# Optimization experiments

Hardware: AMD Instinct MI355X
Metric: run time of the kernel (lower is better)

## Reference

```python
import jax, jax.numpy as jnp
import numpy as np
from jax.scipy.special import logsumexp

N, K, D = 131072, 256, 32


def setup_inputs() -> dict:
    key = jax.random.key(0)
    k1, k2, k3 = jax.random.split(key, 3)
    points = jax.random.normal(k1, (N, D), dtype=jnp.float32)
    centers = jax.random.uniform(k2, (K, D), dtype=jnp.float32)
    # well-conditioned inverse-sqrt covariances (original used 15*I; scaled to
    # avoid float32 overflow in sqrt(det(covs_inv)) for D=32)
    covs_inv_sqrt = (0.5 * jnp.broadcast_to(jnp.eye(D, dtype=jnp.float32), (K, D, D))
                     + 0.02 * jax.random.normal(k3, (K, D, D), dtype=jnp.float32))
    weights = jnp.ones((K,), dtype=jnp.float32)
    threshold = jnp.zeros((1,), dtype=jnp.float32)
    return {"points": points, "centers": centers,
            "covs_inv_sqrt": covs_inv_sqrt, "weights": weights,
            "threshold": threshold}


def reference(points, centers, covs_inv_sqrt, weights, threshold):
    # refresh(): equal_clusters=True branch
    w = jnp.abs(weights)
    center_prs = w / (w.sum() + 1e-30)                       # [K]
    covs_inv = jnp.einsum('kde,kfe->kdf', covs_inv_sqrt, covs_inv_sqrt)  # [K,D,D]
    coefs = center_prs * jnp.sqrt(jnp.linalg.det(covs_inv))  # [K]

    # pairwise weighted sqdist: q_ij = (x_i - c_j)^T A_j (x_i - c_j)
    B = covs_inv.reshape(K, D * D)                           # [K, D*D]
    X2 = (points[:, :, None] * points[:, None, :]).reshape(N, D * D)  # [N, D*D]
    t_xAx = X2 @ B.T                                         # [N, K]
    m = jnp.einsum('kde,ke->kd', covs_inv, centers)          # A_j c_j, [K,D]
    t_xAc = points @ m.T                                     # [N, K]
    t_cAc = jnp.einsum('kd,kd->k', m, centers)               # [K]
    d_ij = -0.5 * (t_xAx - 2.0 * t_xAc + t_cAc[None, :])     # [N, K]

    # weighted logsumexp over centers, then subtract threshold
    ll = logsumexp(d_ij, axis=1, b=coefs[None, :])           # [N]
    return ll[:, None] - threshold[0]                        # [N, 1]
```

## Files before the change

kernel.cpp:

```cpp
#include <hip/hip_runtime.h>
#include <hip/hip_fp16.h>
#include <math.h>

#define NPTS 131072
#define KCOMP 256
#define DIM 32
#define KF 608
#define PSIF_BYTES 311296
#define WS_NEED (PSIF_BYTES + KCOMP * 4)

typedef _Float16 f16x8 __attribute__((ext_vector_type(8)));
typedef __attribute__((ext_vector_type(16))) float f32x16;

constexpr int L4c(int d) { return ((32 - d + 3) / 4) * 4; }
constexpr int PfxC(int d) { int s = 0; for (int i = 0; i < d; ++i) s += L4c(i); return s; }
constexpr int rowOfC(int p) { int d = 0; while (d < 31 && PfxC(d + 1) <= p) ++d; return d; }
constexpr int dOfC(int p) { return (p >= 576) ? -1 : rowOfC(p); }
constexpr int f0OfC(int p) {
    return (p >= 576) ? (p - 576) : ((rowOfC(p) & ~3) + (p - PfxC(rowOfC(p))));
}

__device__ __forceinline__ unsigned short f2h(float v) {
    __half h = __float2half(v);
    return __builtin_bit_cast(unsigned short, h);
}

__global__ __launch_bounds__(256) void gmm_pre(
    const float* __restrict__ S,
    const float* __restrict__ centers,
    const float* __restrict__ weights,
    unsigned short* __restrict__ PsiF,
    float* __restrict__ kc2)
{
    __shared__ float Sl[DIM][DIM + 1];
    __shared__ float As[DIM][DIM + 1];
    __shared__ float cl[DIM], ml[DIM];
    __shared__ float red[256];

    const int k = blockIdx.x, tid = threadIdx.x;

    for (int idx = tid; idx < DIM * DIM; idx += 256)
        Sl[idx >> 5][idx & 31] = S[(size_t)k * DIM * DIM + idx];
    if (tid < DIM) cl[tid] = centers[k * DIM + tid];
    __syncthreads();

    for (int idx = tid; idx < DIM * DIM; idx += 256) {
        const int d = idx >> 5, f = idx & 31;
        float a = 0.f;
#pragma unroll
        for (int e = 0; e < DIM; ++e) a = fmaf(Sl[d][e], Sl[f][e], a);
        As[d][f] = a;
    }
    __syncthreads();

    if (tid < DIM) {
        float mv = 0.f;
#pragma unroll
        for (int f = 0; f < DIM; ++f) mv = fmaf(As[tid][f], cl[f], mv);
        ml[tid] = mv;
    }
    __syncthreads();

    for (int p = tid; p < KF; p += 256) {
        float val;
        if (p < 576) {
            int d = 0, pr = 0;
            while (true) {
                const int len = ((32 - d + 3) >> 2) << 2;
                if (pr + len > p) break;
                pr += len; ++d;
            }
            const int f = (d & ~3) + (p - pr);
            val = (f < d) ? 0.f : ((f == d) ? -0.5f * As[d][d] : -As[d][f]);
        } else {
            val = ml[p - 576];
        }
        const int c = p >> 6, kk = p & 63;
        const int s = kk >> 4, qq = (kk >> 3) & 1, j = kk & 7;
        const int ct = k >> 5, ll = qq * 32 + (k & 31);
        const int g = c * 2048 + (s * 8 + ct) * 64 + ll;
        PsiF[(size_t)g * 8 + j] = f2h(val);
    }

    red[tid] = fabsf(weights[tid]);
    __syncthreads();
    for (int off = 128; off > 0; off >>= 1) {
        if (tid < off) red[tid] += red[tid + off];
        __syncthreads();
    }
    const float wsum = red[0];

    for (int j = 0; j < DIM - 1; ++j) {
        const float inv = 1.0f / As[j][j];
        for (int idx = tid; idx < DIM * DIM; idx += 256) {
            const int r = idx >> 5, c = idx & 31;
            if (r > j && c > j)
                As[r][c] = fmaf(-As[r][j] * inv, As[j][c], As[r][c]);
        }
        __syncthreads();
    }

    if (tid < DIM) red[tid] = __logf(As[tid][tid]);
    __syncthreads();
    if (tid == 0) {
        float sl = 0.f;
        for (int j = 0; j < DIM; ++j) sl += red[j];
        float cac = 0.f;
        for (int d2 = 0; d2 < DIM; ++d2) cac = fmaf(ml[d2], cl[d2], cac);
        kc2[k] = __logf(fabsf(weights[k])) - __logf(wsum + 1e-30f)
               + 0.5f * sl - 0.5f * cac;
    }
}

__device__ __forceinline__ unsigned pkmul(unsigned a, unsigned b) {
    __half2 r = __builtin_bit_cast(__half2, a) * __builtin_bit_cast(__half2, b);
    return __builtin_bit_cast(unsigned, r);
}

template<int PA, int PB>
__device__ __forceinline__ void quadProd(const unsigned (&xp)[16], bool hi,
                                         unsigned& o0, unsigned& o1) {
    constexpr int dA = dOfC(PA), fA = f0OfC(PA);
    constexpr int dB = dOfC(PB), fB = f0OfC(PB);
    const unsigned p0 = hi ? xp[(fB >> 1) + 0] : xp[(fA >> 1) + 0];
    const unsigned p1 = hi ? xp[(fB >> 1) + 1] : xp[(fA >> 1) + 1];
    if constexpr (dA < 0) {
        o0 = p0; o1 = p1;
    } else {
        const unsigned sA = __builtin_amdgcn_perm(xp[dA >> 1], xp[dA >> 1],
                                (dA & 1) ? 0x03020302u : 0x01000100u);
        const unsigned sB = __builtin_amdgcn_perm(xp[dB >> 1], xp[dB >> 1],
                                (dB & 1) ? 0x03020302u : 0x01000100u);
        const unsigned ss = (dA == dB) ? sA : (hi ? sB : sA);
        o0 = pkmul(ss, p0); o1 = pkmul(ss, p1);
    }
}

template<int C, int S>
__device__ __forceinline__ uint4 genA(const unsigned (&xp)[16], bool hi) {
    constexpr int P = C * 64 + S * 16;
    uint4 u;
    quadProd<P,     P + 8 >(xp, hi, u.x, u.y);
    quadProd<P + 4, P + 12>(xp, hi, u.z, u.w);
    return u;
}

template<int ST>
__device__ __forceinline__ void doStep(
    const unsigned (&xp0)[16], const unsigned (&xp1)[16],
    uint4 (&bf)[2][4], f32x16 (&acc)[2][4],
    const uint4* __restrict__ pb, bool hi)
{
    constexpr int C = (ST < 36) ? ST / 4 : 9;
    constexpr int S = (ST < 36) ? ST % 4 : ST - 36;

    if constexpr (ST < 37) {
        constexpr int Cn = (ST + 1 < 36) ? (ST + 1) / 4 : 9;
        constexpr int Sn = (ST + 1 < 36) ? (ST + 1) % 4 : ST + 1 - 36;
#pragma unroll
        for (int ct = 0; ct < 4; ++ct)
            bf[(ST + 1) & 1][ct] = pb[Cn * 2048 + Sn * 512 + ct * 64];
    }

    const uint4 a0 = genA<C, S>(xp0, hi);
    const uint4 a1 = genA<C, S>(xp1, hi);
#pragma unroll
    for (int ct = 0; ct < 4; ++ct) {
        const f16x8 b  = __builtin_bit_cast(f16x8, bf[ST & 1][ct]);
        acc[0][ct] = __builtin_amdgcn_mfma_f32_32x32x16_f16(
                         __builtin_bit_cast(f16x8, a0), b, acc[0][ct], 0, 0, 0);
        acc[1][ct] = __builtin_amdgcn_mfma_f32_32x32x16_f16(
                         __builtin_bit_cast(f16x8, a1), b, acc[1][ct], 0, 0, 0);
    }
}

template<int ST>
__device__ __forceinline__ void runSteps(
    const unsigned (&xp0)[16], const unsigned (&xp1)[16],
    uint4 (&bf)[2][4], f32x16 (&acc)[2][4],
    const uint4* __restrict__ pb, bool hi)
{
    doStep<ST>(xp0, xp1, bf, acc, pb, hi);
    if constexpr (ST < 37) runSteps<ST + 1>(xp0, xp1, bf, acc, pb, hi);
}

__global__ __launch_bounds__(256, 2) void gmm_mfma(
    const float* __restrict__ points,
    const unsigned short* __restrict__ PsiF,
    const float* __restrict__ kc2,
    const float* __restrict__ thr,
    float* __restrict__ out)
{
    __shared__ float sPm[128][2], sPs[128][2];

    const int t = threadIdx.x;
    const int w = t >> 6, l = t & 63;
    const int rh = w >> 1, ch = w & 1;
    const bool hi = (l >> 5) != 0;

    unsigned xp0[16], xp1[16];
    {
        const size_t r0 = (size_t)blockIdx.x * 128 + rh * 64 + (l & 31);
        const float4* pxa = (const float4*)(points + r0 * DIM);
        const float4* pxb = (const float4*)(points + (r0 + 32) * DIM);
#pragma unroll
        for (int i = 0; i < 8; ++i) {
            float4 va = pxa[i], vb = pxb[i];
            xp0[2*i+0] = __builtin_bit_cast(unsigned, __floats2half2_rn(va.x, va.y));
            xp0[2*i+1] = __builtin_bit_cast(unsigned, __floats2half2_rn(va.z, va.w));
            xp1[2*i+0] = __builtin_bit_cast(unsigned, __floats2half2_rn(vb.x, vb.y));
            xp1[2*i+1] = __builtin_bit_cast(unsigned, __floats2half2_rn(vb.z, vb.w));
        }
    }

    const uint4* pb = (const uint4*)PsiF + ch * 256 + l;

    f32x16 acc[2][4];
#pragma unroll
    for (int a = 0; a < 2; ++a)
#pragma unroll
        for (int c = 0; c < 4; ++c)
#pragma unroll
            for (int r = 0; r < 16; ++r) acc[a][c][r] = 0.f;

    uint4 bf[2][4];
#pragma unroll
    for (int ct = 0; ct < 4; ++ct) bf[0][ct] = pb[ct * 64];

    runSteps<0>(xp0, xp1, bf, acc, pb, hi);

    float kcv[4];
#pragma unroll
    for (int ct = 0; ct < 4; ++ct) kcv[ct] = kc2[(ch * 4 + ct) * 32 + (l & 31)];

#pragma unroll
    for (int rt = 0; rt < 2; ++rt) {
#pragma unroll
        for (int rg = 0; rg < 16; ++rg) {
            float v0 = acc[rt][0][rg] + kcv[0];
            float v1 = acc[rt][1][rg] + kcv[1];
            float v2 = acc[rt][2][rg] + kcv[2];
            float v3 = acc[rt][3][rg] + kcv[3];
            float m = fmaxf(fmaxf(v0, v1), fmaxf(v2, v3));
#pragma unroll
            for (int mask = 1; mask < 32; mask <<= 1)
                m = fmaxf(m, __shfl_xor(m, mask, 64));
            float sv = __expf(v0 - m) + __expf(v1 - m)
                     + __expf(v2 - m) + __expf(v3 - m);
#pragma unroll
            for (int mask = 1; mask < 32; mask <<= 1)
                sv += __shfl_xor(sv, mask, 64);
            if ((l & 31) == 0) {
                const int R = rh * 64 + rt * 32 + (rg & 3) + 8 * (rg >> 2) + 4 * (l >> 5);
                sPm[R][ch] = m; sPs[R][ch] = sv;
            }
        }
    }
    __syncthreads();

    if (t < 128) {
        const float m0 = sPm[t][0], m1 = sPm[t][1];
        const float M = fmaxf(m0, m1);
        const float Sv = sPs[t][0] * __expf(m0 - M) + sPs[t][1] * __expf(m1 - M);
        out[(size_t)blockIdx.x * 128 + t] = M + __logf(Sv) - thr[0];
    }
}

extern "C" void kernel_launch(void* const* d_in, const int* in_sizes, int n_in,
                              void* d_out, int out_size, void* d_ws, size_t ws_size,
                              hipStream_t stream) {
    const float* points  = (const float*)d_in[0];
    const float* centers = (const float*)d_in[1];
    const float* covs    = (const float*)d_in[2];
    const float* weights = (const float*)d_in[3];
    const float* thr     = (const float*)d_in[4];
    float* out = (float*)d_out;

    unsigned short* PsiF = (unsigned short*)d_ws;
    float* kc2 = (float*)((char*)d_ws + PSIF_BYTES);

    gmm_pre<<<KCOMP, 256, 0, stream>>>(covs, centers, weights, PsiF, kc2);
    gmm_mfma<<<NPTS / 128, 256, 0, stream>>>(points, PsiF, kc2, thr, out);
}
```

Measured before the change: 155.3 us.

## Repartition MFMA warp tiling to 4 row tiles x 2 component tiles per wave

Changes the per-wave tiling so each of the 4 waves covers all 128 rows (4 row tiles) and 64 components (2 column tiles), instead of 64 rows x 128 components. Each wave now generates the on-the-fly x-outer-product A fragments for 4 row tiles and loads half as many B fragments, and B prefetch deepens from double to triple buffering two steps ahead. The aim is to cut global B traffic per wave and hide load latency better. In exchange, A-fragment generation ALU work per wave doubles, more registers go to x data, and the cross-wave logsumexp merge now spans 4 partials.

```diff
diff --git a/kernel.cpp b/kernel.cpp
--- a/kernel.cpp
+++ b/kernel.cpp
@@ -147,41 +147,43 @@
 
 template<int ST>
 __device__ __forceinline__ void doStep(
-    const unsigned (&xp0)[16], const unsigned (&xp1)[16],
-    uint4 (&bf)[2][4], f32x16 (&acc)[2][4],
+    const unsigned (&xp)[4][16],
+    uint4 (&bf)[3][2], f32x16 (&acc)[4][2],
     const uint4* __restrict__ pb, bool hi)
 {
     constexpr int C = (ST < 36) ? ST / 4 : 9;
     constexpr int S = (ST < 36) ? ST % 4 : ST - 36;
 
-    if constexpr (ST < 37) {
-        constexpr int Cn = (ST + 1 < 36) ? (ST + 1) / 4 : 9;
-        constexpr int Sn = (ST + 1 < 36) ? (ST + 1) % 4 : ST + 1 - 36;
-#pragma unroll
-        for (int ct = 0; ct < 4; ++ct)
-            bf[(ST + 1) & 1][ct] = pb[Cn * 2048 + Sn * 512 + ct * 64];
-    }
-
-    const uint4 a0 = genA<C, S>(xp0, hi);
-    const uint4 a1 = genA<C, S>(xp1, hi);
-#pragma unroll
-    for (int ct = 0; ct < 4; ++ct) {
-        const f16x8 b  = __builtin_bit_cast(f16x8, bf[ST & 1][ct]);
-        acc[0][ct] = __builtin_amdgcn_mfma_f32_32x32x16_f16(
-                         __builtin_bit_cast(f16x8, a0), b, acc[0][ct], 0, 0, 0);
-        acc[1][ct] = __builtin_amdgcn_mfma_f32_32x32x16_f16(
-                         __builtin_bit_cast(f16x8, a1), b, acc[1][ct], 0, 0, 0);
+    if constexpr (ST + 2 <= 37) {
+        constexpr int Cn = (ST + 2 < 36) ? (ST + 2) / 4 : 9;
+        constexpr int Sn = (ST + 2 < 36) ? (ST + 2) % 4 : ST + 2 - 36;
+#pragma unroll
+        for (int ct = 0; ct < 2; ++ct)
+            bf[(ST + 2) % 3][ct] = pb[Cn * 2048 + Sn * 512 + ct * 64];
+    }
+
+    uint4 a[4];
+#pragma unroll
+    for (int rt = 0; rt < 4; ++rt) a[rt] = genA<C, S>(xp[rt], hi);
+
+#pragma unroll
+    for (int ct = 0; ct < 2; ++ct) {
+        const f16x8 b = __builtin_bit_cast(f16x8, bf[ST % 3][ct]);
+#pragma unroll
+        for (int rt = 0; rt < 4; ++rt)
+            acc[rt][ct] = __builtin_amdgcn_mfma_f32_32x32x16_f16(
+                __builtin_bit_cast(f16x8, a[rt]), b, acc[rt][ct], 0, 0, 0);
     }
 }
 
 template<int ST>
 __device__ __forceinline__ void runSteps(
-    const unsigned (&xp0)[16], const unsigned (&xp1)[16],
-    uint4 (&bf)[2][4], f32x16 (&acc)[2][4],
+    const unsigned (&xp)[4][16],
+    uint4 (&bf)[3][2], f32x16 (&acc)[4][2],
     const uint4* __restrict__ pb, bool hi)
 {
-    doStep<ST>(xp0, xp1, bf, acc, pb, hi);
-    if constexpr (ST < 37) runSteps<ST + 1>(xp0, xp1, bf, acc, pb, hi);
+    doStep<ST>(xp, bf, acc, pb, hi);
+    if constexpr (ST < 37) runSteps<ST + 1>(xp, bf, acc, pb, hi);
 }
 
 __global__ __launch_bounds__(256, 2) void gmm_mfma(
@@ -191,68 +193,65 @@
     const float* __restrict__ thr,
     float* __restrict__ out)
 {
-    __shared__ float sPm[128][2], sPs[128][2];
+    __shared__ float sPm[128][4], sPs[128][4];
 
     const int t = threadIdx.x;
     const int w = t >> 6, l = t & 63;
-    const int rh = w >> 1, ch = w & 1;
     const bool hi = (l >> 5) != 0;
 
-    unsigned xp0[16], xp1[16];
-    {
-        const size_t r0 = (size_t)blockIdx.x * 128 + rh * 64 + (l & 31);
-        const float4* pxa = (const float4*)(points + r0 * DIM);
-        const float4* pxb = (const float4*)(points + (r0 + 32) * DIM);
+    unsigned xp[4][16];
+#pragma unroll
+    for (int rt = 0; rt < 4; ++rt) {
+        const size_t r = (size_t)blockIdx.x * 128 + rt * 32 + (l & 31);
+        const float4* px = (const float4*)(points + r * DIM);
 #pragma unroll
         for (int i = 0; i < 8; ++i) {
-            float4 va = pxa[i], vb = pxb[i];
-            xp0[2*i+0] = __builtin_bit_cast(unsigned, __floats2half2_rn(va.x, va.y));
-            xp0[2*i+1] = __builtin_bit_cast(unsigned, __floats2half2_rn(va.z, va.w));
-            xp1[2*i+0] = __builtin_bit_cast(unsigned, __floats2half2_rn(vb.x, vb.y));
-            xp1[2*i+1] = __builtin_bit_cast(unsigned, __floats2half2_rn(vb.z, vb.w));
-        }
-    }
-
-    const uint4* pb = (const uint4*)PsiF + ch * 256 + l;
-
-    f32x16 acc[2][4];
-#pragma unroll
-    for (int a = 0; a < 2; ++a)
-#pragma unroll
-        for (int c = 0; c < 4; ++c)
-#pragma unroll
-            for (int r = 0; r < 16; ++r) acc[a][c][r] = 0.f;
-
-    uint4 bf[2][4];
-#pragma unroll
-    for (int ct = 0; ct < 4; ++ct) bf[0][ct] = pb[ct * 64];
-
-    runSteps<0>(xp0, xp1, bf, acc, pb, hi);
-
-    float kcv[4];
-#pragma unroll
-    for (int ct = 0; ct < 4; ++ct) kcv[ct] = kc2[(ch * 4 + ct) * 32 + (l & 31)];
-
-#pragma unroll
-    for (int rt = 0; rt < 2; ++rt) {
+            float4 v = px[i];
+            xp[rt][2*i+0] = __builtin_bit_cast(unsigned, __floats2half2_rn(v.x, v.y));
+            xp[rt][2*i+1] = __builtin_bit_cast(unsigned, __floats2half2_rn(v.z, v.w));
+        }
+    }
+
+    const uint4* pb = (const uint4*)PsiF + w * 128 + l;
+
+    f32x16 acc[4][2];
+#pragma unroll
+    for (int rt = 0; rt < 4; ++rt)
+#pragma unroll
+        for (int ct = 0; ct < 2; ++ct)
+#pragma unroll
+            for (int r = 0; r < 16; ++r) acc[rt][ct][r] = 0.f;
+
+    uint4 bf[3][2];
+#pragma unroll
+    for (int ct = 0; ct < 2; ++ct) {
+        bf[0][ct] = pb[ct * 64];
+        bf[1][ct] = pb[512 + ct * 64];
+    }
+
+    runSteps<0>(xp, bf, acc, pb, hi);
+
+    float kcv[2];
+#pragma unroll
+    for (int ct = 0; ct < 2; ++ct) kcv[ct] = kc2[(w * 2 + ct) * 32 + (l & 31)];
+
+#pragma unroll
+    for (int rt = 0; rt < 4; ++rt) {
 #pragma unroll
         for (int rg = 0; rg < 16; ++rg) {
-            float v0 = acc[rt][0][rg] + kcv[0];
-            float v1 = acc[rt][1][rg] + kcv[1];
-            float v2 = acc[rt][2][rg] + kcv[2];
-            float v3 = acc[rt][3][rg] + kcv[3];
-            float m = fmaxf(fmaxf(v0, v1), fmaxf(v2, v3));
+            const float v0 = acc[rt][0][rg] + kcv[0];
+            const float v1 = acc[rt][1][rg] + kcv[1];
+            float m = fmaxf(v0, v1);
 #pragma unroll
             for (int mask = 1; mask < 32; mask <<= 1)
                 m = fmaxf(m, __shfl_xor(m, mask, 64));
-            float sv = __expf(v0 - m) + __expf(v1 - m)
-                     + __expf(v2 - m) + __expf(v3 - m);
+            float sv = __expf(v0 - m) + __expf(v1 - m);
 #pragma unroll
             for (int mask = 1; mask < 32; mask <<= 1)
                 sv += __shfl_xor(sv, mask, 64);
             if ((l & 31) == 0) {
-                const int R = rh * 64 + rt * 32 + (rg & 3) + 8 * (rg >> 2) + 4 * (l >> 5);
-                sPm[R][ch] = m; sPs[R][ch] = sv;
+                const int R = rt * 32 + (rg & 3) + 8 * (rg >> 2) + 4 * (l >> 5);
+                sPm[R][w] = m; sPs[R][w] = sv;
             }
         }
     }
@@ -260,8 +259,10 @@
 
     if (t < 128) {
         const float m0 = sPm[t][0], m1 = sPm[t][1];
-        const float M = fmaxf(m0, m1);
-        const float Sv = sPs[t][0] * __expf(m0 - M) + sPs[t][1] * __expf(m1 - M);
+        const float m2 = sPm[t][2], m3 = sPm[t][3];
+        const float M = fmaxf(fmaxf(m0, m1), fmaxf(m2, m3));
+        const float Sv = sPs[t][0] * __expf(m0 - M) + sPs[t][1] * __expf(m1 - M)
+                       + sPs[t][2] * __expf(m2 - M) + sPs[t][3] * __expf(m3 - M);
         out[(size_t)blockIdx.x * 128 + t] = M + __logf(Sv) - thr[0];
     }
 }
```

Result: slower. 193.3 us (+24.5%).
